# Kernel tuning notes

Hardware: AMD Instinct MI355X
Metric: run time of the kernel (lower is better)

The kernel has to match this reference:

```python
import jax, jax.numpy as jnp
import numpy as np

D_MODEL = 1024
N_HEADS = 16
D_FF = 4096
EPS = 1e-5


def setup_inputs() -> dict:
    key = jax.random.key(0)
    ks = jax.random.split(key, 13)
    d, f = D_MODEL, D_FF
    s = 1.0 / np.sqrt(d)
    sf = 1.0 / np.sqrt(f)
    return {
        "x": jax.random.normal(ks[0], (2, 2048, d), dtype=jnp.float32),
        "Wq": jax.random.normal(ks[1], (d, d), dtype=jnp.float32) * s,
        "bq": jnp.zeros((d,), jnp.float32),
        "Wk": jax.random.normal(ks[2], (d, d), dtype=jnp.float32) * s,
        "bk": jnp.zeros((d,), jnp.float32),
        "Wv": jax.random.normal(ks[3], (d, d), dtype=jnp.float32) * s,
        "bv": jnp.zeros((d,), jnp.float32),
        "Wo": jax.random.normal(ks[4], (d, d), dtype=jnp.float32) * s,
        "bo": jnp.zeros((d,), jnp.float32),
        "W1": jax.random.normal(ks[5], (f, d), dtype=jnp.float32) * s,
        "b1": jnp.zeros((f,), jnp.float32),
        "W2": jax.random.normal(ks[6], (d, f), dtype=jnp.float32) * sf,
        "b2": jnp.zeros((d,), jnp.float32),
        "g1": jnp.ones((d,), jnp.float32),
        "be1": jnp.zeros((d,), jnp.float32),
        "g2": jnp.ones((d,), jnp.float32),
        "be2": jnp.zeros((d,), jnp.float32),
    }


def _layernorm(x, g, b):
    mu = jnp.mean(x, axis=-1, keepdims=True)
    var = jnp.mean(jnp.square(x - mu), axis=-1, keepdims=True)
    return (x - mu) * jax.lax.rsqrt(var + EPS) * g + b


def reference(x, Wq, bq, Wk, bk, Wv, bv, Wo, bo, W1, b1, W2, b2, g1, be1, g2, be2):
    B, S, D = x.shape
    H = N_HEADS
    dk = D // H
    # QKV projections (torch Linear: x @ W.T + b), reshape to [B,H,S,dk]
    def proj(W, b):
        return (x @ W.T + b).reshape(B, S, H, dk).transpose(0, 2, 1, 3)
    Q, K, V = proj(Wq, bq), proj(Wk, bk), proj(Wv, bv)
    scores = jnp.einsum("bhsd,bhtd->bhst", Q, K) / jnp.sqrt(jnp.float32(dk))
    attn = jax.nn.softmax(scores, axis=-1)
    ctx = jnp.einsum("bhst,bhtd->bhsd", attn, V)
    ctx = ctx.transpose(0, 2, 1, 3).reshape(B, S, D)
    attn_out = ctx @ Wo.T + bo
    x1 = _layernorm(x + attn_out, g1, be1)
    ff = jax.nn.relu(x1 @ W1.T + b1) @ W2.T + b2
    return _layernorm(x1 + ff, g2, be2)
```

## Files before the change

kernel.cpp:

```cpp
#include <hip/hip_runtime.h>

typedef unsigned short u16;
typedef unsigned int u32;
typedef unsigned long long u64;
typedef __attribute__((ext_vector_type(8))) short short8;
typedef __attribute__((ext_vector_type(4))) float f32x4;

#define D_MODEL 1024
#define SEQ 2048
#define NH 16
#define DK 64
#define DFF 4096
#define NTOK 4096
#define LOG2E 1.44269504f

__device__ __forceinline__ u16 f2bf(float f) {
    unsigned x = __builtin_bit_cast(unsigned, f);
    x = x + 0x7fffu + ((x >> 16) & 1u);
    return (u16)(x >> 16);
}

__device__ __forceinline__ float bf2f(u16 v) {
    return __builtin_bit_cast(float, (u32)v << 16);
}

__device__ __forceinline__ float fexp2(float x) {
    float r;
    asm("v_exp_f32 %0, %1" : "=v"(r) : "v"(x));
    return r;
}

__device__ __forceinline__ void gload_lds16(const void* g, void* l) {
    __builtin_amdgcn_global_load_lds(
        (__attribute__((address_space(1))) void*)g,
        (__attribute__((address_space(3))) void*)l, 16, 0, 0);
}

__device__ __forceinline__ void cvt_body(const float* __restrict__ in,
                                         u16* __restrict__ out, int blk) {
    size_t i = ((size_t)blk * 256 + threadIdx.x) * 4;
    float4 v = *(const float4*)(in + i);
    out[i + 0] = f2bf(v.x);
    out[i + 1] = f2bf(v.y);
    out[i + 2] = f2bf(v.z);
    out[i + 3] = f2bf(v.w);
}

__global__ __launch_bounds__(256) void cvt_bf16_x4(
    const float* __restrict__ sx, const float* __restrict__ s0,
    const float* __restrict__ s1, const float* __restrict__ s2,
    const float* __restrict__ s3, u16* __restrict__ dx, u16* __restrict__ d0,
    u16* __restrict__ d1, u16* __restrict__ d2, u16* __restrict__ d3) {
    int f = blockIdx.x;
    if (f < 4096) {
        cvt_body(sx, dx, f);
    } else {
        int which = (f - 4096) >> 10, blk = (f - 4096) & 1023;
        const float* s = which == 0 ? s0 : which == 1 ? s1 : which == 2 ? s2 : s3;
        u16* d = which == 0 ? d0 : which == 1 ? d1 : which == 2 ? d2 : d3;
        cvt_body(s, d, blk);
    }
}

__global__ __launch_bounds__(256) void cvt_bf16_2(
    const float* __restrict__ s0, const float* __restrict__ s1,
    u16* __restrict__ d0, u16* __restrict__ d1) {
    int which = blockIdx.x >> 12, blk = blockIdx.x & 4095;
    cvt_body(which ? s1 : s0, which ? d1 : d0, blk);
}

template <int BM, int BN>
__device__ __forceinline__ void gemm_acc(const u16* __restrict__ A,
                                         const u16* __restrict__ W,
                                         int K, int m0, int n0,
                                         f32x4 (&acc)[BM / 32][BN / 32]) {
    constexpr int MR = BM / 32, NR = BN / 32;
    __shared__ short8 As[2][BM / 2][8];
    __shared__ short8 Bs[2][BN / 2][8];
    const int tid = threadIdx.x;
    const int lane = tid & 63, w = tid >> 6;
    const int l15 = lane & 15, lg = lane >> 4;
    const int wr = (w >> 1) * (BM / 2), wc = (w & 1) * (BN / 2);
    const int pswA = l15 >> 1;
    const int cbase = ((l15 & 1) << 2) + lg;

#pragma unroll
    for (int i = 0; i < MR; ++i)
#pragma unroll
        for (int j = 0; j < NR; ++j) acc[i][j] = (f32x4){0.f, 0.f, 0.f, 0.f};

#define STAGE_AB(B_, K0)                                                       \
    {                                                                          \
        _Pragma("unroll") for (int j = 0; j < BM / 64; ++j) {                  \
            int idx = j * 256 + tid;                                           \
            int prow = idx >> 3;                                               \
            int s = (idx & 7) ^ (prow & 7);                                    \
            int lrow = prow * 2 + (s >> 2), lc = s & 3;                        \
            gload_lds16(A + (size_t)(m0 + lrow) * K + (K0) + lc * 8,           \
                        (char*)As[B_] + (j * 256 + w * 64) * 16);              \
        }                                                                      \
        _Pragma("unroll") for (int j = 0; j < BN / 64; ++j) {                  \
            int idx = j * 256 + tid;                                           \
            int prow = idx >> 3;                                               \
            int s = (idx & 7) ^ (prow & 7);                                    \
            int lrow = prow * 2 + (s >> 2), lc = s & 3;                        \
            gload_lds16(W + (size_t)(n0 + lrow) * K + (K0) + lc * 8,           \
                        (char*)Bs[B_] + (j * 256 + w * 64) * 16);              \
        }                                                                      \
    }
#define COMPUTE(B_)                                                            \
    {                                                                          \
        short8 af[MR], bf[NR];                                                 \
        _Pragma("unroll") for (int m = 0; m < MR; ++m)                         \
            af[m] = As[B_][(wr + m * 16) / 2 + (l15 >> 1)][cbase ^ pswA];      \
        _Pragma("unroll") for (int n = 0; n < NR; ++n)                         \
            bf[n] = Bs[B_][(wc + n * 16) / 2 + (l15 >> 1)][cbase ^ pswA];      \
        _Pragma("unroll") for (int m = 0; m < MR; ++m)                         \
            _Pragma("unroll") for (int n = 0; n < NR; ++n)                     \
                acc[m][n] = __builtin_amdgcn_mfma_f32_16x16x32_bf16(           \
                    af[m], bf[n], acc[m][n], 0, 0, 0);                         \
    }

    STAGE_AB(0, 0);
    for (int k0 = 0; k0 < K; k0 += 64) {
        __syncthreads();
        STAGE_AB(1, k0 + 32);
        COMPUTE(0);
        __syncthreads();
        if (k0 + 64 < K) STAGE_AB(0, k0 + 64);
        COMPUTE(1);
    }
#undef STAGE_AB
#undef COMPUTE
}

template <int BM, int BN, int EPI, int XCD>
__global__ __launch_bounds__(256) void gemm_bt(
    const u16* __restrict__ A, const u16* __restrict__ W,
    const float* __restrict__ bias, u16* __restrict__ outb,
    float* __restrict__ outf, int M, int N, int K) {
    int m0, n0;
    if (XCD) {
        int f = blockIdx.x;
        int xcd = f & 7, j = f >> 3;
        int mq = xcd >> 1, nh = xcd & 1;
        int mi = j & 7, ni = j >> 3;
        m0 = (mq * 8 + mi) * BM;
        n0 = (nh * 16 + ni) * BN;
    } else {
        m0 = blockIdx.y * BM;
        n0 = blockIdx.x * BN;
    }
    f32x4 acc[BM / 32][BN / 32];
    gemm_acc<BM, BN>(A, W, K, m0, n0, acc);
    const int lane = threadIdx.x & 63, w = threadIdx.x >> 6;
    const int l15 = lane & 15, lg = lane >> 4;
    const int wr = (w >> 1) * (BM / 2), wc = (w & 1) * (BN / 2);
#pragma unroll
    for (int m = 0; m < BM / 32; ++m)
#pragma unroll
        for (int n = 0; n < BN / 32; ++n) {
            int gn = n0 + wc + n * 16 + l15;
            float bv = bias[gn];
#pragma unroll
            for (int r = 0; r < 4; ++r) {
                int gm = m0 + wr + m * 16 + lg * 4 + r;
                float v = acc[m][n][r] + bv;
                if (EPI == 0) outf[(size_t)gm * N + gn] = v;
                else outb[(size_t)gm * N + gn] = f2bf(fmaxf(v, 0.f));
            }
        }
}

__global__ __launch_bounds__(256) void gemm_k64(
    const u16* __restrict__ A, const u16* __restrict__ W,
    const float* __restrict__ bias, u16* __restrict__ outb,
    u16* __restrict__ outb2, int M, int N, int K, int KZ) {
    __shared__ short8 As[64][8];
    __shared__ short8 Bs[128][8];
    const int tid = threadIdx.x;
    const int lane = tid & 63, w = tid >> 6;
    const int l15 = lane & 15, lg = lane >> 4;
    const int wr = (w >> 1) * 32, wc = (w & 1) * 64;
    const int psw = l15 & 7;
    const int f = blockIdx.x;
    const int xcd = f & 7, j = f >> 3;
    const int mi = j & 7, n = (j >> 3) & 7, kz = j >> 6;
    const int m0 = (xcd * 8 + mi) * 64, n0 = n * 128;
    const int kl = K / KZ, kbase = kz * kl;
    u16* out = kz ? outb2 : outb;

    f32x4 acc[2][4];
#pragma unroll
    for (int i = 0; i < 2; ++i)
#pragma unroll
        for (int jj = 0; jj < 4; ++jj) acc[i][jj] = (f32x4){0.f, 0.f, 0.f, 0.f};

    for (int k0 = kbase; k0 < kbase + kl; k0 += 64) {
        __syncthreads();
#pragma unroll
        for (int jj = 0; jj < 2; ++jj) {
            int idx = jj * 256 + tid;
            int r = idx >> 3, ck = idx & 7;
            gload_lds16(A + (size_t)(m0 + r) * K + k0 + ((ck ^ (r & 7)) * 8),
                        (char*)As + (jj * 256 + w * 64) * 16);
        }
#pragma unroll
        for (int jj = 0; jj < 4; ++jj) {
            int idx = jj * 256 + tid;
            int r = idx >> 3, ck = idx & 7;
            gload_lds16(W + (size_t)(n0 + r) * K + k0 + ((ck ^ (r & 7)) * 8),
                        (char*)Bs + (jj * 256 + w * 64) * 16);
        }
        __syncthreads();

#pragma unroll
        for (int kk = 0; kk < 2; ++kk) {
            short8 af[2], bf[4];
#pragma unroll
            for (int m = 0; m < 2; ++m)
                af[m] = As[wr + m * 16 + l15][(kk * 4 + lg) ^ psw];
#pragma unroll
            for (int nn = 0; nn < 4; ++nn)
                bf[nn] = Bs[wc + nn * 16 + l15][(kk * 4 + lg) ^ psw];
#pragma unroll
            for (int m = 0; m < 2; ++m)
#pragma unroll
                for (int nn = 0; nn < 4; ++nn)
                    acc[m][nn] = __builtin_amdgcn_mfma_f32_16x16x32_bf16(
                        af[m], bf[nn], acc[m][nn], 0, 0, 0);
        }
    }

#pragma unroll
    for (int m = 0; m < 2; ++m)
#pragma unroll
        for (int nn = 0; nn < 4; ++nn) {
            int gn = n0 + wc + nn * 16 + l15;
            float bv = (kz == 0) ? bias[gn] : 0.f;
#pragma unroll
            for (int r = 0; r < 4; ++r) {
                int gm = m0 + wr + m * 16 + lg * 4 + r;
                out[(size_t)gm * N + gn] = f2bf(acc[m][nn][r] + bv);
            }
        }
}

__global__ __launch_bounds__(256) void gemm_qkv(
    const u16* __restrict__ A, const u16* __restrict__ Wq,
    const u16* __restrict__ Wk, const u16* __restrict__ Wv,
    const float* __restrict__ bq, const float* __restrict__ bk,
    const float* __restrict__ bv, u16* __restrict__ Qo, u16* __restrict__ Ko,
    u16* __restrict__ Vo) {
    const int f = blockIdx.x;
    const int xcd = f & 7, j = f >> 3;
    const int mi = j & 3, q = j >> 2;
    const int mat = q >> 3;
    const int m0 = (xcd * 4 + mi) * 128, n0 = (q & 7) * 128;
    const u16* W = mat == 0 ? Wq : (mat == 1 ? Wk : Wv);
    const float* bias = mat == 0 ? bq : (mat == 1 ? bk : bv);
    const float scale = (mat == 0) ? 0.125f * LOG2E : 1.0f;
    f32x4 acc[4][4];
    gemm_acc<128, 128>(A, W, D_MODEL, m0, n0, acc);
    const int lane = threadIdx.x & 63, w = threadIdx.x >> 6;
    const int l15 = lane & 15, lg = lane >> 4;
    const int wr = (w >> 1) * 64, wc = (w & 1) * 64;

    if (mat == 2) {
#pragma unroll
        for (int m = 0; m < 4; ++m)
#pragma unroll
            for (int n = 0; n < 4; ++n) {
                int gn = n0 + wc + n * 16 + l15;
                float bv2 = bias[gn];
                int h = gn >> 6, d = gn & 63;
                int gm0 = m0 + wr + m * 16 + lg * 4;
                int b = gm0 >> 11, s = gm0 & 2047;
                u64 pk = (u64)f2bf(acc[m][n][0] + bv2) |
                         ((u64)f2bf(acc[m][n][1] + bv2) << 16) |
                         ((u64)f2bf(acc[m][n][2] + bv2) << 32) |
                         ((u64)f2bf(acc[m][n][3] + bv2) << 48);
                size_t obase = (size_t)(b * NH + h) * DK * SEQ;
                int soff = (s & ~63) + ((((s >> 3) & 7) ^ (d & 7)) << 3) + (s & 7);
                *(u64*)(Vo + obase + (size_t)d * SEQ + soff) = pk;
            }
    } else {
        u16* out = mat == 0 ? Qo : Ko;
#pragma unroll
        for (int m = 0; m < 4; ++m)
#pragma unroll
            for (int n = 0; n < 4; ++n) {
                int gn = n0 + wc + n * 16 + l15;
                float bv2 = bias[gn];
                int h = gn >> 6, d = gn & 63;
#pragma unroll
                for (int r = 0; r < 4; ++r) {
                    int gm = m0 + wr + m * 16 + lg * 4 + r;
                    int b = gm >> 11, s = gm & 2047;
                    float v = (acc[m][n][r] + bv2) * scale;
                    out[(((size_t)(b * NH + h)) * SEQ + s) * DK + d] = f2bf(v);
                }
            }
    }
}

#define KVB 64
__global__ __launch_bounds__(512) void attn_fwd(const u16* __restrict__ Q,
                                                const u16* __restrict__ Kp,
                                                const u16* __restrict__ Vg_,
                                                u16* __restrict__ ctx) {
    __shared__ __align__(16) u16 Kt[2][64 * 64];
    __shared__ __align__(16) u16 Vt[2][64 * 64];
    __shared__ __align__(16) u16 Ps[8][16 * 64];

    const int tid = threadIdx.x;
    const int lane = tid & 63;
    const int w = tid >> 6;
    const int l15 = lane & 15;
    const int lg = lane >> 4;
    const int f = blockIdx.x + 16 * blockIdx.y;
    const int bh = f & 31;
    const int qblk = f >> 5;
    const int qbase = qblk * 128 + w * 16;
    const u16* Qb = Q + (size_t)bh * SEQ * DK;
    const u16* Kb = Kp + (size_t)bh * SEQ * DK;
    const u16* Vg = Vg_ + (size_t)bh * DK * SEQ;

    short8 qf[2];
#pragma unroll
    for (int hf = 0; hf < 2; ++hf)
        qf[hf] = *(const short8*)(Qb + (size_t)(qbase + l15) * DK + hf * 32 + lg * 8);

    short8 onesf;
#pragma unroll
    for (int e = 0; e < 8; ++e) onesf[e] = (short)0x3F80;

    f32x4 zero = {0.f, 0.f, 0.f, 0.f};
    f32x4 o[4], o1 = zero;
#pragma unroll
    for (int db = 0; db < 4; ++db) o[db] = zero;
    float m_own = 0.f;

    u16* Pu = Ps[w];
    const int psw = l15 & 7;

#define STAGE_V(T0, BUF)                                                       \
    {                                                                          \
        gload_lds16(Vg + (size_t)(tid >> 3) * SEQ + (T0) + (tid & 7) * 8,      \
                    (char*)Vt[BUF] + (w * 64) * 16);                           \
    }
#define STAGE_K(T0, BUF)                                                       \
    {                                                                          \
        int kv = tid >> 3, ck = tid & 7;                                       \
        gload_lds16(Kb + (size_t)((T0) + kv) * DK + ((ck ^ (kv & 7)) * 8),     \
                    (char*)Kt[BUF] + (w * 64) * 16);                           \
    }
#define KF(BUF, NB, HALF)                                                      \
    (*(const short8*)((const char*)Kt[BUF] + ((NB)*16 + l15) * 128 +           \
                      (((((HALF)*4 + lg)) ^ psw) << 4)))

#define ATTN_TILE(BUF)                                                         \
    {                                                                          \
        f32x4 seed = {-m_own, -m_own, -m_own, -m_own};                         \
        f32x4 sc[4];                                                           \
        __builtin_amdgcn_s_setprio(1);                                         \
        _Pragma("unroll") for (int nb = 0; nb < 4; ++nb) {                     \
            sc[nb] = __builtin_amdgcn_mfma_f32_16x16x32_bf16(                  \
                KF(BUF, nb, 0), qf[0], seed, 0, 0, 0);                         \
            sc[nb] = __builtin_amdgcn_mfma_f32_16x16x32_bf16(                  \
                KF(BUF, nb, 1), qf[1], sc[nb], 0, 0, 0);                       \
        }                                                                      \
        __builtin_amdgcn_s_setprio(0);                                         \
        float a0 = fmaxf(fmaxf(sc[0][0], sc[0][1]), sc[0][2]);                 \
        float a1 = fmaxf(fmaxf(sc[0][3], sc[1][0]), sc[1][1]);                 \
        float a2 = fmaxf(fmaxf(sc[1][2], sc[1][3]), sc[2][0]);                 \
        float a3 = fmaxf(fmaxf(sc[2][1], sc[2][2]), sc[2][3]);                 \
        float a4 = fmaxf(fmaxf(sc[3][0], sc[3][1]), sc[3][2]);                 \
        float lm = fmaxf(fmaxf(fmaxf(a0, a1), a2),                             \
                         fmaxf(fmaxf(a3, a4), sc[3][3]));                      \
        if (__any(lm > 8.f)) {                                                 \
            float rv = fmaxf(lm, __shfl_xor(lm, 16));                          \
            rv = fmaxf(rv, __shfl_xor(rv, 32));                                \
            float rvp = fmaxf(rv, 0.f);                                        \
            float fac = fexp2(-rvp);                                           \
            m_own += rvp;                                                      \
            _Pragma("unroll") for (int nb = 0; nb < 4; ++nb)                   \
                _Pragma("unroll") for (int r = 0; r < 4; ++r)                  \
                    sc[nb][r] -= rvp;                                          \
            _Pragma("unroll") for (int r = 0; r < 4; ++r) {                    \
                float fr = __shfl(fac, lg * 4 + r);                            \
                o1[r] *= fr;                                                   \
                _Pragma("unroll") for (int db = 0; db < 4; ++db)               \
                    o[db][r] *= fr;                                            \
            }                                                                  \
        }                                                                      \
        _Pragma("unroll") for (int nb = 0; nb < 4; ++nb) {                     \
            float p0 = fexp2(sc[nb][0]);                                       \
            float p1 = fexp2(sc[nb][1]);                                       \
            float p2 = fexp2(sc[nb][2]);                                       \
            float p3 = fexp2(sc[nb][3]);                                       \
            u32 pk01 = __builtin_amdgcn_perm(__builtin_bit_cast(u32, p1),      \
                                             __builtin_bit_cast(u32, p0),      \
                                             0x07060302u);                     \
            u32 pk23 = __builtin_amdgcn_perm(__builtin_bit_cast(u32, p3),      \
                                             __builtin_bit_cast(u32, p2),      \
                                             0x07060302u);                     \
            int ck = (nb * 2 + (lg >> 1)) ^ psw;                               \
            u64* dst = (u64*)(Pu + l15 * 64 + ck * 8 + (lg & 1) * 4);          \
            *dst = (u64)pk01 | ((u64)pk23 << 32);                              \
        }                                                                      \
        short8 pa[2];                                                          \
        _Pragma("unroll") for (int ts = 0; ts < 2; ++ts)                       \
            pa[ts] = *(const short8*)(Pu + l15 * 64 + (((ts * 4 + lg) ^ psw) * 8)); \
        __builtin_amdgcn_s_setprio(1);                                         \
        _Pragma("unroll") for (int db = 0; db < 4; ++db) {                     \
            const int d = db * 16 + l15;                                       \
            _Pragma("unroll") for (int ts = 0; ts < 2; ++ts) {                 \
                short8 vb = *(const short8*)((const char*)Vt[BUF] + d * 128 +  \
                                             (((ts * 4 + lg) ^ psw) << 4));    \
                o[db] = __builtin_amdgcn_mfma_f32_16x16x32_bf16(               \
                    pa[ts], vb, o[db], 0, 0, 0);                               \
            }                                                                  \
        }                                                                      \
        o1 = __builtin_amdgcn_mfma_f32_16x16x32_bf16(pa[0], onesf, o1, 0, 0, 0); \
        o1 = __builtin_amdgcn_mfma_f32_16x16x32_bf16(pa[1], onesf, o1, 0, 0, 0); \
        __builtin_amdgcn_s_setprio(0);                                         \
    }

    STAGE_K(0, 0);
    STAGE_V(0, 0);

    for (int t0 = 0; t0 < SEQ; t0 += 2 * KVB) {
        __syncthreads();
        STAGE_K(t0 + KVB, 1);
        STAGE_V(t0 + KVB, 1);
        ATTN_TILE(0);
        __syncthreads();
        if (t0 + 2 * KVB < SEQ) {
            STAGE_K(t0 + 2 * KVB, 0);
            STAGE_V(t0 + 2 * KVB, 0);
        }
        ATTN_TILE(1);
    }

    const int b = bh >> 4, h = bh & 15;
#pragma unroll
    for (int r = 0; r < 4; ++r) {
        float inv = 1.0f / o1[r];
        int srow = qbase + lg * 4 + r;
        size_t rowoff = ((size_t)(b * SEQ + srow)) * D_MODEL + h * DK;
#pragma unroll
        for (int db = 0; db < 4; ++db)
            ctx[rowoff + db * 16 + l15] = f2bf(o[db][r] * inv);
    }
#undef STAGE_V
#undef STAGE_K
#undef KF
#undef ATTN_TILE
}

__global__ __launch_bounds__(256) void ln_res(const float* __restrict__ X,
                                              const u16* __restrict__ Y,
                                              const u16* __restrict__ Y2,
                                              const float* __restrict__ gamma,
                                              const float* __restrict__ beta,
                                              float* __restrict__ outf,
                                              u16* __restrict__ outb) {
    __shared__ float red[8];
    const int row = blockIdx.x, t = threadIdx.x;
    const size_t off = (size_t)row * D_MODEL + t * 4;
    float4 xv = *(const float4*)(X + off);
    ushort4 yv = *(const ushort4*)(Y + off);
    float sx = xv.x + bf2f(yv.x), sy = xv.y + bf2f(yv.y);
    float sz = xv.z + bf2f(yv.z), sw = xv.w + bf2f(yv.w);
    if (Y2) {
        ushort4 y2 = *(const ushort4*)(Y2 + off);
        sx += bf2f(y2.x); sy += bf2f(y2.y); sz += bf2f(y2.z); sw += bf2f(y2.w);
    }
    float ps = sx + sy + sz + sw;
#pragma unroll
    for (int o2 = 32; o2; o2 >>= 1) ps += __shfl_xor(ps, o2);
    if ((t & 63) == 0) red[t >> 6] = ps;
    __syncthreads();
    float mu = (red[0] + red[1] + red[2] + red[3]) * (1.0f / D_MODEL);
    float d0 = sx - mu, d1 = sy - mu, d2 = sz - mu, d3 = sw - mu;
    float p2 = d0 * d0 + d1 * d1 + d2 * d2 + d3 * d3;
#pragma unroll
    for (int o2 = 32; o2; o2 >>= 1) p2 += __shfl_xor(p2, o2);
    if ((t & 63) == 0) red[4 + (t >> 6)] = p2;
    __syncthreads();
    float var = (red[4] + red[5] + red[6] + red[7]) * (1.0f / D_MODEL);
    float rstd = rsqrtf(var + 1e-5f);
    float4 gv = *(const float4*)(gamma + t * 4);
    float4 bv = *(const float4*)(beta + t * 4);
    float r0 = d0 * rstd * gv.x + bv.x;
    float r1 = d1 * rstd * gv.y + bv.y;
    float r2 = d2 * rstd * gv.z + bv.z;
    float r3 = d3 * rstd * gv.w + bv.w;
    float4 res; res.x = r0; res.y = r1; res.z = r2; res.w = r3;
    *(float4*)(outf + off) = res;
    if (outb) {
        outb[off + 0] = f2bf(r0);
        outb[off + 1] = f2bf(r1);
        outb[off + 2] = f2bf(r2);
        outb[off + 3] = f2bf(r3);
    }
}

extern "C" void kernel_launch(void* const* d_in, const int* in_sizes, int n_in,
                              void* d_out, int out_size, void* d_ws, size_t ws_size,
                              hipStream_t stream) {
    (void)in_sizes; (void)n_in; (void)out_size; (void)ws_size;
    const float* x  = (const float*)d_in[0];
    const float* Wq = (const float*)d_in[1];
    const float* bq = (const float*)d_in[2];
    const float* Wk = (const float*)d_in[3];
    const float* bk = (const float*)d_in[4];
    const float* Wv = (const float*)d_in[5];
    const float* bv = (const float*)d_in[6];
    const float* Wo = (const float*)d_in[7];
    const float* bo = (const float*)d_in[8];
    const float* W1 = (const float*)d_in[9];
    const float* b1 = (const float*)d_in[10];
    const float* W2 = (const float*)d_in[11];
    const float* b2 = (const float*)d_in[12];
    const float* g1 = (const float*)d_in[13];
    const float* be1 = (const float*)d_in[14];
    const float* g2 = (const float*)d_in[15];
    const float* be2 = (const float*)d_in[16];

    char* ws = (char*)d_ws;
    u16* xb   = (u16*)(ws);
    u16* Qb   = (u16*)(ws + ((size_t)8 << 20));
    u16* Kb   = (u16*)(ws + ((size_t)16 << 20));
    u16* Vb   = (u16*)(ws + ((size_t)24 << 20));
    float* x1 = (float*)(ws + ((size_t)32 << 20));
    u16* Fs   = (u16*)(ws + ((size_t)48 << 20));
    u16* Fs2  = (u16*)(ws + ((size_t)56 << 20));
    u16* hb   = (u16*)(ws + ((size_t)64 << 20));
    u16* Wqb = hb;
    u16* Wkb = hb + (1u << 20);
    u16* Wvb = hb + (2u << 20);
    u16* Wob = hb + (3u << 20);
    u16* W1b = Qb;
    u16* W2b = Kb;
    u16* Vtg = Fs;
    u16* ctxb = xb;
    u16* x1b  = Vb;

    cvt_bf16_x4<<<dim3(8192), 256, 0, stream>>>(x, Wq, Wk, Wv, Wo,
                                                xb, Wqb, Wkb, Wvb, Wob);

    gemm_qkv<<<dim3(768), 256, 0, stream>>>(xb, Wqb, Wkb, Wvb, bq, bk, bv,
                                            Qb, Kb, Vtg);

    attn_fwd<<<dim3(SEQ / 128, 32), 512, 0, stream>>>(Qb, Kb, Vtg, ctxb);

    cvt_bf16_2<<<dim3(8192), 256, 0, stream>>>(W1, W2, W1b, W2b);

    gemm_k64<<<dim3(512), 256, 0, stream>>>(ctxb, Wob, bo, Fs, nullptr,
                                            NTOK, D_MODEL, D_MODEL, 1);

    ln_res<<<dim3(NTOK), 256, 0, stream>>>(x, Fs, nullptr, g1, be1, x1, x1b);

    gemm_bt<128, 128, 1, 1><<<dim3(1024), 256, 0, stream>>>(
        x1b, W1b, b1, hb, nullptr, NTOK, DFF, D_MODEL);

    gemm_k64<<<dim3(1024), 256, 0, stream>>>(hb, W2b, b2, Fs, Fs2,
                                             NTOK, D_MODEL, DFF, 2);

    ln_res<<<dim3(NTOK), 256, 0, stream>>>(x1, Fs, Fs2, g2, be2,
                                           (float*)d_out, nullptr);
}
```

Before: 255.4 us.

## Merge weight conversions, widen attention KV tile, drop fp32 x1 buffer

All weight and input fp32-to-bf16 conversions now run in one launch, removing the separate W1/W2 conversion kernel. The attention kernel stages 128 keys/values per buffer instead of 64, halving the number of barriers and staging rounds per sequence pass at the cost of doubled LDS usage. The first layernorm no longer writes an fp32 copy of x1; the second layernorm reads the bf16 copy instead, which cuts memory traffic but makes the residual path use bf16-rounded values.

```diff
diff --git a/kernel.cpp b/kernel.cpp
--- a/kernel.cpp
+++ b/kernel.cpp
@@ -46,27 +46,26 @@
     out[i + 3] = f2bf(v.w);
 }
 
-__global__ __launch_bounds__(256) void cvt_bf16_x4(
+__global__ __launch_bounds__(256) void cvt_all(
     const float* __restrict__ sx, const float* __restrict__ s0,
     const float* __restrict__ s1, const float* __restrict__ s2,
-    const float* __restrict__ s3, u16* __restrict__ dx, u16* __restrict__ d0,
-    u16* __restrict__ d1, u16* __restrict__ d2, u16* __restrict__ d3) {
+    const float* __restrict__ s3, const float* __restrict__ s4,
+    const float* __restrict__ s5, u16* __restrict__ dx, u16* __restrict__ d0,
+    u16* __restrict__ d1, u16* __restrict__ d2, u16* __restrict__ d3,
+    u16* __restrict__ d4, u16* __restrict__ d5) {
     int f = blockIdx.x;
     if (f < 4096) {
         cvt_body(sx, dx, f);
-    } else {
+    } else if (f < 8192) {
         int which = (f - 4096) >> 10, blk = (f - 4096) & 1023;
         const float* s = which == 0 ? s0 : which == 1 ? s1 : which == 2 ? s2 : s3;
         u16* d = which == 0 ? d0 : which == 1 ? d1 : which == 2 ? d2 : d3;
         cvt_body(s, d, blk);
-    }
-}
-
-__global__ __launch_bounds__(256) void cvt_bf16_2(
-    const float* __restrict__ s0, const float* __restrict__ s1,
-    u16* __restrict__ d0, u16* __restrict__ d1) {
-    int which = blockIdx.x >> 12, blk = blockIdx.x & 4095;
-    cvt_body(which ? s1 : s0, which ? d1 : d0, blk);
+    } else if (f < 12288) {
+        cvt_body(s4, d4, f - 8192);
+    } else {
+        cvt_body(s5, d5, f - 12288);
+    }
 }
 
 template <int BM, int BN>
@@ -304,13 +303,12 @@
     }
 }
 
-#define KVB 64
 __global__ __launch_bounds__(512) void attn_fwd(const u16* __restrict__ Q,
                                                 const u16* __restrict__ Kp,
                                                 const u16* __restrict__ Vg_,
                                                 u16* __restrict__ ctx) {
-    __shared__ __align__(16) u16 Kt[2][64 * 64];
-    __shared__ __align__(16) u16 Vt[2][64 * 64];
+    __shared__ __align__(16) u16 Kt[2][128 * 64];
+    __shared__ __align__(16) u16 Vt[2][64 * 128];
     __shared__ __align__(16) u16 Ps[8][16 * 64];
 
     const int tid = threadIdx.x;
@@ -346,29 +344,35 @@
 
 #define STAGE_V(T0, BUF)                                                       \
     {                                                                          \
-        gload_lds16(Vg + (size_t)(tid >> 3) * SEQ + (T0) + (tid & 7) * 8,      \
-                    (char*)Vt[BUF] + (w * 64) * 16);                           \
+        _Pragma("unroll") for (int j = 0; j < 2; ++j) {                        \
+            int idx = j * 512 + tid;                                           \
+            gload_lds16(Vg + (size_t)(idx >> 4) * SEQ + (T0) + (idx & 15) * 8, \
+                        (char*)Vt[BUF] + (j * 512 + w * 64) * 16);             \
+        }                                                                      \
     }
 #define STAGE_K(T0, BUF)                                                       \
     {                                                                          \
-        int kv = tid >> 3, ck = tid & 7;                                       \
-        gload_lds16(Kb + (size_t)((T0) + kv) * DK + ((ck ^ (kv & 7)) * 8),     \
-                    (char*)Kt[BUF] + (w * 64) * 16);                           \
-    }
-#define KF(BUF, NB, HALF)                                                      \
-    (*(const short8*)((const char*)Kt[BUF] + ((NB)*16 + l15) * 128 +           \
+        _Pragma("unroll") for (int j = 0; j < 2; ++j) {                        \
+            int idx = j * 512 + tid;                                           \
+            int kv = idx >> 3, ck = idx & 7;                                   \
+            gload_lds16(Kb + (size_t)((T0) + kv) * DK + ((ck ^ (kv & 7)) * 8), \
+                        (char*)Kt[BUF] + (j * 512 + w * 64) * 16);             \
+        }                                                                      \
+    }
+#define KF(BUF, H, NB, HALF)                                                   \
+    (*(const short8*)((const char*)Kt[BUF] + ((H)*64 + (NB)*16 + l15) * 128 +  \
                       (((((HALF)*4 + lg)) ^ psw) << 4)))
 
-#define ATTN_TILE(BUF)                                                         \
+#define ATTN_TILE(BUF, H)                                                      \
     {                                                                          \
         f32x4 seed = {-m_own, -m_own, -m_own, -m_own};                         \
         f32x4 sc[4];                                                           \
         __builtin_amdgcn_s_setprio(1);                                         \
         _Pragma("unroll") for (int nb = 0; nb < 4; ++nb) {                     \
             sc[nb] = __builtin_amdgcn_mfma_f32_16x16x32_bf16(                  \
-                KF(BUF, nb, 0), qf[0], seed, 0, 0, 0);                         \
+                KF(BUF, H, nb, 0), qf[0], seed, 0, 0, 0);                      \
             sc[nb] = __builtin_amdgcn_mfma_f32_16x16x32_bf16(                  \
-                KF(BUF, nb, 1), qf[1], sc[nb], 0, 0, 0);                       \
+                KF(BUF, H, nb, 1), qf[1], sc[nb], 0, 0, 0);                    \
         }                                                                      \
         __builtin_amdgcn_s_setprio(0);                                         \
         float a0 = fmaxf(fmaxf(sc[0][0], sc[0][1]), sc[0][2]);                 \
@@ -416,8 +420,8 @@
         _Pragma("unroll") for (int db = 0; db < 4; ++db) {                     \
             const int d = db * 16 + l15;                                       \
             _Pragma("unroll") for (int ts = 0; ts < 2; ++ts) {                 \
-                short8 vb = *(const short8*)((const char*)Vt[BUF] + d * 128 +  \
-                                             (((ts * 4 + lg) ^ psw) << 4));    \
+                short8 vb = *(const short8*)((const char*)Vt[BUF] + d * 256 +  \
+                                             (((H)*8 + (((ts * 4 + lg) ^ psw))) << 4)); \
                 o[db] = __builtin_amdgcn_mfma_f32_16x16x32_bf16(               \
                     pa[ts], vb, o[db], 0, 0, 0);                               \
             }                                                                  \
@@ -430,17 +434,19 @@
     STAGE_K(0, 0);
     STAGE_V(0, 0);
 
-    for (int t0 = 0; t0 < SEQ; t0 += 2 * KVB) {
+    for (int t0 = 0; t0 < SEQ; t0 += 256) {
         __syncthreads();
-        STAGE_K(t0 + KVB, 1);
-        STAGE_V(t0 + KVB, 1);
-        ATTN_TILE(0);
+        STAGE_K(t0 + 128, 1);
+        STAGE_V(t0 + 128, 1);
+        ATTN_TILE(0, 0);
+        ATTN_TILE(0, 1);
         __syncthreads();
-        if (t0 + 2 * KVB < SEQ) {
-            STAGE_K(t0 + 2 * KVB, 0);
-            STAGE_V(t0 + 2 * KVB, 0);
+        if (t0 + 256 < SEQ) {
+            STAGE_K(t0 + 256, 0);
+            STAGE_V(t0 + 256, 0);
         }
-        ATTN_TILE(1);
+        ATTN_TILE(1, 0);
+        ATTN_TILE(1, 1);
     }
 
     const int b = bh >> 4, h = bh & 15;
@@ -459,7 +465,8 @@
 #undef ATTN_TILE
 }
 
-__global__ __launch_bounds__(256) void ln_res(const float* __restrict__ X,
+template <bool XBF>
+__global__ __launch_bounds__(256) void ln_res(const void* __restrict__ Xv,
                                               const u16* __restrict__ Y,
                                               const u16* __restrict__ Y2,
                                               const float* __restrict__ gamma,
@@ -469,10 +476,17 @@
     __shared__ float red[8];
     const int row = blockIdx.x, t = threadIdx.x;
     const size_t off = (size_t)row * D_MODEL + t * 4;
-    float4 xv = *(const float4*)(X + off);
+    float x0, x1_, x2, x3;
+    if (XBF) {
+        ushort4 xv = *(const ushort4*)((const u16*)Xv + off);
+        x0 = bf2f(xv.x); x1_ = bf2f(xv.y); x2 = bf2f(xv.z); x3 = bf2f(xv.w);
+    } else {
+        float4 xv = *(const float4*)((const float*)Xv + off);
+        x0 = xv.x; x1_ = xv.y; x2 = xv.z; x3 = xv.w;
+    }
     ushort4 yv = *(const ushort4*)(Y + off);
-    float sx = xv.x + bf2f(yv.x), sy = xv.y + bf2f(yv.y);
-    float sz = xv.z + bf2f(yv.z), sw = xv.w + bf2f(yv.w);
+    float sx = x0 + bf2f(yv.x), sy = x1_ + bf2f(yv.y);
+    float sz = x2 + bf2f(yv.z), sw = x3 + bf2f(yv.w);
     if (Y2) {
         ushort4 y2 = *(const ushort4*)(Y2 + off);
         sx += bf2f(y2.x); sy += bf2f(y2.y); sz += bf2f(y2.z); sw += bf2f(y2.w);
@@ -497,8 +511,10 @@
     float r1 = d1 * rstd * gv.y + bv.y;
     float r2 = d2 * rstd * gv.z + bv.z;
     float r3 = d3 * rstd * gv.w + bv.w;
-    float4 res; res.x = r0; res.y = r1; res.z = r2; res.w = r3;
-    *(float4*)(outf + off) = res;
+    if (outf) {
+        float4 res; res.x = r0; res.y = r1; res.z = r2; res.w = r3;
+        *(float4*)(outf + off) = res;
+    }
     if (outb) {
         outb[off + 0] = f2bf(r0);
         outb[off + 1] = f2bf(r1);
@@ -533,8 +549,9 @@
     u16* xb   = (u16*)(ws);
     u16* Qb   = (u16*)(ws + ((size_t)8 << 20));
     u16* Kb   = (u16*)(ws + ((size_t)16 << 20));
-    u16* Vb   = (u16*)(ws + ((size_t)24 << 20));
-    float* x1 = (float*)(ws + ((size_t)32 << 20));
+    u16* x1b  = (u16*)(ws + ((size_t)24 << 20));
+    u16* W1b  = (u16*)(ws + ((size_t)32 << 20));
+    u16* W2b  = (u16*)(ws + ((size_t)40 << 20));
     u16* Fs   = (u16*)(ws + ((size_t)48 << 20));
     u16* Fs2  = (u16*)(ws + ((size_t)56 << 20));
     u16* hb   = (u16*)(ws + ((size_t)64 << 20));
@@ -542,26 +559,22 @@
     u16* Wkb = hb + (1u << 20);
     u16* Wvb = hb + (2u << 20);
     u16* Wob = hb + (3u << 20);
-    u16* W1b = Qb;
-    u16* W2b = Kb;
     u16* Vtg = Fs;
     u16* ctxb = xb;
-    u16* x1b  = Vb;
-
-    cvt_bf16_x4<<<dim3(8192), 256, 0, stream>>>(x, Wq, Wk, Wv, Wo,
-                                                xb, Wqb, Wkb, Wvb, Wob);
+
+    cvt_all<<<dim3(16384), 256, 0, stream>>>(x, Wq, Wk, Wv, Wo, W1, W2,
+                                             xb, Wqb, Wkb, Wvb, Wob, W1b, W2b);
 
     gemm_qkv<<<dim3(768), 256, 0, stream>>>(xb, Wqb, Wkb, Wvb, bq, bk, bv,
                                             Qb, Kb, Vtg);
 
     attn_fwd<<<dim3(SEQ / 128, 32), 512, 0, stream>>>(Qb, Kb, Vtg, ctxb);
 
-    cvt_bf16_2<<<dim3(8192), 256, 0, stream>>>(W1, W2, W1b, W2b);
-
     gemm_k64<<<dim3(512), 256, 0, stream>>>(ctxb, Wob, bo, Fs, nullptr,
                                             NTOK, D_MODEL, D_MODEL, 1);
 
-    ln_res<<<dim3(NTOK), 256, 0, stream>>>(x, Fs, nullptr, g1, be1, x1, x1b);
+    ln_res<false><<<dim3(NTOK), 256, 0, stream>>>(x, Fs, nullptr, g1, be1,
+                                                  nullptr, x1b);
 
     gemm_bt<128, 128, 1, 1><<<dim3(1024), 256, 0, stream>>>(
         x1b, W1b, b1, hb, nullptr, NTOK, DFF, D_MODEL);
@@ -569,6 +582,6 @@
     gemm_k64<<<dim3(1024), 256, 0, stream>>>(hb, W2b, b2, Fs, Fs2,
                                              NTOK, D_MODEL, DFF, 2);
 
-    ln_res<<<dim3(NTOK), 256, 0, stream>>>(x1, Fs, Fs2, g2, be2,
-                                           (float*)d_out, nullptr);
-}
+    ln_res<true><<<dim3(NTOK), 256, 0, stream>>>(x1b, Fs, Fs2, g2, be2,
+                                                 (float*)d_out, nullptr);
+}
```

After: 254.4 us. About the same (-0.4%).
